# Kernel tuning notes

Measured on AMD Instinct MI355X. Metric: run time of the kernel, lower is better.

## Reference

```python
import jax, jax.numpy as jnp
import numpy as np

V, E, L, T, H, B = 8124, 1024, 24, 512, 16, 2
S = E // H
DFF = E * 8 // 3  # 2730
EPS = 1e-5
SCALE = 1.0 / np.sqrt(E)  # note: 1/sqrt(emb_dim), as in the source


def _pe():
    # sinusoidal positional encoding [T, E]
    pos = jnp.arange(T, dtype=jnp.float32)[:, None]
    div = jnp.exp(jnp.arange(0, E, 2, dtype=jnp.float32) * (-np.log(10000.0) / E))
    pe = jnp.zeros((T, E), jnp.float32)
    pe = pe.at[:, 0::2].set(jnp.sin(pos * div))
    pe = pe.at[:, 1::2].set(jnp.cos(pos * div))
    return pe


def _rms(x, g):
    # NOTE: source takes the mean over the WHOLE tensor (no dim arg)
    rms = jnp.sqrt(jnp.mean(x.astype(jnp.float32) ** 2) + EPS)
    return (x / rms * g).astype(x.dtype)


def setup_inputs() -> dict:
    key = jax.random.key(0)
    ks = jax.random.split(key, 9)
    def w(k, shape):
        return jax.random.normal(k, shape, jnp.float32) * 0.02
    return {
        "tokens": jax.random.randint(ks[0], (B, T), 0, V),
        "emb_table": w(ks[1], (V, E)),
        "Wqkv": w(ks[2], (L, E, 3 * E)), "bqkv": jnp.zeros((L, 3 * E), jnp.float32),
        "Wo": w(ks[3], (L, E, E)), "bo": jnp.zeros((L, E), jnp.float32),
        "W1": w(ks[4], (L, E, DFF)), "b1": jnp.zeros((L, DFF), jnp.float32),
        "W3": w(ks[5], (L, E, DFF)), "b3": jnp.zeros((L, DFF), jnp.float32),
        "W2": w(ks[6], (L, DFF, E)), "b2": jnp.zeros((L, E), jnp.float32),
        "g_mha": jnp.ones((L, E), jnp.float32),
        "g_ff": jnp.ones((L, E), jnp.float32),
        "g_final": jnp.ones((E,), jnp.float32),
        "Wout": w(ks[7], (E, V)), "bout": jnp.zeros((V,), jnp.float32),
    }


def reference(tokens, emb_table, Wqkv, bqkv, Wo, bo, W1, b1, W3, b3, W2, b2,
              g_mha, g_ff, g_final, Wout, bout):
    x = emb_table[tokens] + _pe()[None]  # [B,T,E]
    mask = jnp.tril(jnp.ones((T, T), bool))

    def block(x, p):
        wqkv, bq, wo, bo_, w1, b1_, w3, b3_, w2, b2_, gm, gf = p
        # --- causal MHA ---
        y = _rms(x, gm)
        qkv = (y @ wqkv + bq).reshape(B, T, H, 3, S)
        q = qkv[..., 0, :].transpose(0, 2, 1, 3)  # [B,H,T,S]
        k = qkv[..., 1, :].transpose(0, 2, 1, 3)
        v = qkv[..., 2, :].transpose(0, 2, 1, 3)
        attn = jnp.einsum('bhqd,bhkd->bhqk', q, k).astype(jnp.float32) * SCALE
        attn = jnp.where(mask, attn, -jnp.inf)
        attn = jax.nn.softmax(attn, axis=-1).astype(x.dtype)
        y = jnp.einsum('bhqk,bhkd->bhqd', attn, v)
        y = y.transpose(0, 2, 1, 3).reshape(B, T, E)
        x = x + (y @ wo + bo_)
        # --- SwiGLU FFN ---
        h = _rms(x, gf)
        u = h @ w1 + b1_
        u = u * jax.nn.sigmoid(u) * (h @ w3 + b3_)
        return x + (u @ w2 + b2_), None

    x, _ = jax.lax.scan(block, x, (Wqkv, bqkv, Wo, bo, W1, b1, W3, b3, W2, b2, g_mha, g_ff))
    return _rms(x, g_final) @ Wout + bout  # [B,T,V]
```

## Files before the change

### kernel.cpp

```cpp
#include <hip/hip_runtime.h>
#include <hip/hip_bf16.h>
#include <math.h>

#define EDIM   1024
#define TSEQ   512
#define NBATCH 2
#define NHEAD  16
#define HDIM   64
#define NLAYER 24
#define VOCAB  8124
#define DFFDIM 2730
#define DPAD   2752
#define MTOK   (NBATCH*TSEQ)
#define NELEM  (MTOK*EDIM)
#define EPSF   1e-5f
#define SCALEF (1.0f/32.0f)
#define NEGBIG (-1e30f)

typedef __bf16 bf16x8 __attribute__((ext_vector_type(8)));
typedef __bf16 bf16x4 __attribute__((ext_vector_type(4)));
typedef float  f32x4  __attribute__((ext_vector_type(4)));

#define MFMA(a, b, c) __builtin_amdgcn_mfma_f32_16x16x32_bf16((a), (b), (c), 0, 0, 0)

__device__ __forceinline__ void gl_lds16(const __bf16* g, __bf16* l) {
  __builtin_amdgcn_global_load_lds(
      (const __attribute__((address_space(1))) void*)g,
      (__attribute__((address_space(3))) void*)l, 16, 0, 0);
}
template <int N> __device__ __forceinline__ void vmwait() {
  asm volatile("s_waitcnt vmcnt(%0)" :: "n"(N) : "memory");
}
__device__ __forceinline__ void lgkm_barrier() {
  asm volatile("s_waitcnt lgkmcnt(0)" ::: "memory");
  __builtin_amdgcn_s_barrier();
}

__global__ __launch_bounds__(256) void k_embed(const int* __restrict__ tok,
                                               const float* __restrict__ emb,
                                               float* __restrict__ x) {
  const int bt = blockIdx.x;
  const int t  = bt & (TSEQ - 1);
  const int tk = tok[bt];
  const float* er = emb + (size_t)tk * EDIM;
  float* xr = x + (size_t)bt * EDIM;
  for (int e = threadIdx.x * 4; e < EDIM; e += 256 * 4) {
    float4 v = *(const float4*)(er + e);
    float vv[4] = {v.x, v.y, v.z, v.w};
    float ou[4];
#pragma unroll
    for (int j = 0; j < 4; ++j) {
      int ee = e + j;
      int i2 = ee & ~1;
      float freq = expf(-(float)i2 * (9.210340371976184f / 1024.0f));
      float ang  = (float)t * freq;
      ou[j] = vv[j] + ((ee & 1) ? cosf(ang) : sinf(ang));
    }
    *(float4*)(xr + e) = make_float4(ou[0], ou[1], ou[2], ou[3]);
  }
}

__global__ __launch_bounds__(256) void k_red1f(float* __restrict__ x,
                                               const float* __restrict__ pb,
                                               int np,
                                               const float* __restrict__ bias,
                                               float* __restrict__ part) {
  float s = 0.f;
  const bool fold = (pb != nullptr);
  for (int i = (blockIdx.x * 256 + threadIdx.x) * 4; i < NELEM; i += 256 * 256 * 4) {
    float4 v = *(const float4*)(x + i);
    if (fold) {
      for (int z = 0; z < np; ++z) {
        float4 a = *(const float4*)(pb + (size_t)z * NELEM + i);
        v.x += a.x; v.y += a.y; v.z += a.z; v.w += a.w;
      }
      float4 c = *(const float4*)(bias + (i & (EDIM - 1)));
      v.x += c.x; v.y += c.y; v.z += c.z; v.w += c.w;
      *(float4*)(x + i) = v;
    }
    s += v.x * v.x + v.y * v.y + v.z * v.z + v.w * v.w;
  }
#pragma unroll
  for (int o = 32; o > 0; o >>= 1) s += __shfl_down(s, o);
  __shared__ float sm[4];
  if ((threadIdx.x & 63) == 0) sm[threadIdx.x >> 6] = s;
  __syncthreads();
  if (threadIdx.x == 0) part[blockIdx.x] = sm[0] + sm[1] + sm[2] + sm[3];
}

__device__ __forceinline__ void conv_tile(const float* __restrict__ src,
                                          const float* __restrict__ gk,
                                          __bf16* __restrict__ dst,
                                          int K, int N, int Kpad, int tk, int tn) {
  __shared__ float st[64][65];
  const int k0 = tk << 6, n0 = tn << 6;
  const int tid = threadIdx.x;
  {
    const int r0 = tid >> 4, c4 = (tid & 15) << 2;
#pragma unroll
    for (int i = 0; i < 4; ++i) {
      const int r = r0 + i * 16;
      const int k = k0 + r;
      float4 v = make_float4(0.f, 0.f, 0.f, 0.f);
      if (k < K) {
        const float* sp = src + (size_t)k * N + n0 + c4;
        if (n0 + c4 + 3 < N) v = *(const float4*)sp;
        else {
          if (n0 + c4 + 0 < N) v.x = sp[0];
          if (n0 + c4 + 1 < N) v.y = sp[1];
          if (n0 + c4 + 2 < N) v.z = sp[2];
          if (n0 + c4 + 3 < N) v.w = sp[3];
        }
        if (gk) {
          const float gv = gk[k];
          v.x *= gv; v.y *= gv; v.z *= gv; v.w *= gv;
        }
      }
      st[r][c4 + 0] = v.x; st[r][c4 + 1] = v.y; st[r][c4 + 2] = v.z; st[r][c4 + 3] = v.w;
    }
  }
  __syncthreads();
  {
    const int nl0 = tid >> 3, c8 = (tid & 7) << 3;
#pragma unroll
    for (int i = 0; i < 2; ++i) {
      const int nl = nl0 + i * 32;
      bf16x8 o = {(__bf16)st[c8 + 0][nl], (__bf16)st[c8 + 1][nl],
                  (__bf16)st[c8 + 2][nl], (__bf16)st[c8 + 3][nl],
                  (__bf16)st[c8 + 4][nl], (__bf16)st[c8 + 5][nl],
                  (__bf16)st[c8 + 6][nl], (__bf16)st[c8 + 7][nl]};
      *(bf16x8*)&dst[(size_t)(n0 + nl) * Kpad + k0 + c8] = o;
    }
  }
}

__global__ __launch_bounds__(256) void k_convAll(const float* __restrict__ Wqkv,
                                                 const float* __restrict__ Wo,
                                                 const float* __restrict__ W1,
                                                 const float* __restrict__ W3,
                                                 const float* __restrict__ W2w,
                                                 const float* __restrict__ g_mha,
                                                 const float* __restrict__ g_ff,
                                                 __bf16* qkvT, __bf16* woT,
                                                 __bf16* w1T, __bf16* w3T, __bf16* w2T) {
  int b = blockIdx.x;
  const int l = b / 3088; b -= l * 3088;
  if (b < 768) {
    conv_tile(Wqkv + (size_t)l * 1024 * 3072, g_mha + (size_t)l * EDIM,
              qkvT + (size_t)l * 3072 * 1024, 1024, 3072, 1024, b / 48, b % 48);
  } else if (b < 1024) {
    int t = b - 768;
    conv_tile(Wo + (size_t)l * 1024 * 1024, nullptr,
              woT + (size_t)l * 1024 * 1024, 1024, 1024, 1024, t / 16, t % 16);
  } else if (b < 1712) {
    int t = b - 1024;
    conv_tile(W1 + (size_t)l * 1024 * DFFDIM, g_ff + (size_t)l * EDIM,
              w1T + (size_t)l * DPAD * 1024, 1024, DFFDIM, 1024, t / 43, t % 43);
  } else if (b < 2400) {
    int t = b - 1712;
    conv_tile(W3 + (size_t)l * 1024 * DFFDIM, g_ff + (size_t)l * EDIM,
              w3T + (size_t)l * DPAD * 1024, 1024, DFFDIM, 1024, t / 43, t % 43);
  } else {
    int t = b - 2400;
    conv_tile(W2w + (size_t)l * DFFDIM * 1024, nullptr,
              w2T + (size_t)l * 1024 * DPAD, DFFDIM, 1024, DPAD, t / 16, t % 16);
  }
}

__global__ __launch_bounds__(256) void k_convH(const float* __restrict__ Wout,
                                               const float* __restrict__ g_final,
                                               __bf16* __restrict__ WoutT) {
  conv_tile(Wout, g_final, WoutT, 1024, VOCAB, 1024, blockIdx.x >> 7, blockIdx.x & 127);
}

template <int BN, int MODE, int FUSE>
__global__ __launch_bounds__(256) void mm(
    const __bf16* __restrict__ A, const float* __restrict__ Af,
    const __bf16* __restrict__ B0w, const __bf16* __restrict__ B1w,
    const float* __restrict__ bias0, const float* __restrict__ bias1,
    const float* __restrict__ part,
    float* __restrict__ po, __bf16* __restrict__ ob,
    __bf16* __restrict__ qout, __bf16* __restrict__ kout, __bf16* __restrict__ vout,
    int N, int lda, int ldb, int Ktot) {
  constexpr int DUAL = (MODE == 2) ? 2 : 1;
  constexpr int FN = BN / 32;
  constexpr int BL = (BN == 128) ? 4 : 2 * DUAL;
  __shared__ __bf16 As[2][8][128][8];
  __shared__ __bf16 Bs[2][DUAL][8][BN][8];
  const int tid = threadIdx.x, lane = tid & 63, wave = tid >> 6;
  const int m0 = blockIdx.y << 7, n0 = blockIdx.x * BN;
  const int wm0 = (wave >> 1) * 64, wn0 = (wave & 1) * (BN / 2);
  const int lr = lane & 15, kh = lane >> 4;

  const int ktiles = Ktot >> 6;
  const int nt0 = (ktiles + gridDim.z - 1) / gridDim.z;
  const int tbeg = blockIdx.z * nt0;
  const int tend = (ktiles < tbeg + nt0) ? ktiles : (tbeg + nt0);
  const int nt = tend - tbeg;

  f32x4 acc[DUAL][4][FN];
#pragma unroll
  for (int d = 0; d < DUAL; ++d)
#pragma unroll
    for (int mi = 0; mi < 4; ++mi)
#pragma unroll
      for (int fn = 0; fn < FN; ++fn) acc[d][mi][fn] = (f32x4){0.f, 0.f, 0.f, 0.f};

  float4 ar[4][2];
  auto LOADA = [&](int t) {
    const int k0 = (tbeg + t) << 6;
#pragma unroll
    for (int i = 0; i < 4; ++i) {
      const int d = i * 256 + tid;
      const int row = d >> 3, kb = d & 7;
      const float* ap = Af + (size_t)(m0 + row) * lda + k0 + kb * 8;
      ar[i][0] = *(const float4*)ap; ar[i][1] = *(const float4*)(ap + 4);
    }
  };
  auto DSWA = [&](int buf) {
#pragma unroll
    for (int i = 0; i < 4; ++i) {
      const int d = i * 256 + tid;
      const int row = d >> 3, kb = d & 7;
      float4 a = ar[i][0], b = ar[i][1];
      bf16x8 w = {(__bf16)a.x, (__bf16)a.y, (__bf16)a.z, (__bf16)a.w,
                  (__bf16)b.x, (__bf16)b.y, (__bf16)b.z, (__bf16)b.w};
      *(bf16x8*)&As[buf][kb][row ^ kb][0] = w;
    }
  };
  auto STAGEA_G = [&](int buf, int t) {
    const int k0 = (tbeg + t) << 6;
#pragma unroll
    for (int i = 0; i < 4; ++i) {
      const int d = i * 256 + tid;
      gl_lds16(A + (size_t)(m0 + (d & 127)) * lda + k0 + (d >> 7) * 8,
               &As[buf][d >> 7][d & 127][0]);
    }
  };
  auto STAGEB = [&](int buf, int t) {
    const int k0 = (tbeg + t) << 6;
    if (BN == 128) {
#pragma unroll
      for (int i = 0; i < 4; ++i) {
        const int d = i * 256 + tid;
        gl_lds16(B0w + (size_t)(n0 + (d & 127)) * ldb + k0 + (d >> 7) * 8,
                 &Bs[buf][0][d >> 7][d & 127][0]);
      }
    } else {
#pragma unroll
      for (int i = 0; i < 2; ++i) {
        const int d = i * 256 + tid;
        gl_lds16(B0w + (size_t)(n0 + (d & 63)) * ldb + k0 + (d >> 6) * 8,
                 &Bs[buf][0][d >> 6][d & 63][0]);
      }
      if (DUAL == 2) {
#pragma unroll
        for (int i = 0; i < 2; ++i) {
          const int d = i * 256 + tid;
          gl_lds16(B1w + (size_t)(n0 + (d & 63)) * ldb + k0 + (d >> 6) * 8,
                   &Bs[buf][DUAL - 1][d >> 6][d & 63][0]);
        }
      }
    }
  };
  auto COMP = [&](int buf) {
#pragma unroll
    for (int ks = 0; ks < 2; ++ks) {
      const int kidx = ks * 4 + kh;
      bf16x8 af[4];
#pragma unroll
      for (int mi = 0; mi < 4; ++mi) {
        const int r = wm0 + mi * 16 + lr;
        af[mi] = *(const bf16x8*)&As[buf][kidx][FUSE ? (r ^ kidx) : r][0];
      }
#pragma unroll
      for (int d = 0; d < DUAL; ++d)
#pragma unroll
        for (int fn = 0; fn < FN; ++fn) {
          bf16x8 bfr = *(const bf16x8*)&Bs[buf][d][kidx][wn0 + fn * 16 + lr][0];
#pragma unroll
          for (int mi = 0; mi < 4; ++mi)
            acc[d][mi][fn] = MFMA(af[mi], bfr, acc[d][mi][fn]);
        }
    }
  };

  int cur = 0;
  if (FUSE) {
    LOADA(0); STAGEB(0, 0); DSWA(0);
    asm volatile("s_waitcnt lgkmcnt(0)" ::: "memory");
    vmwait<0>(); __builtin_amdgcn_s_barrier();
    for (int t = 0; t < nt - 1; ++t) {
      LOADA(t + 1);
      STAGEB(cur ^ 1, t + 1);
      COMP(cur);
      DSWA(cur ^ 1);
      asm volatile("s_waitcnt lgkmcnt(0)" ::: "memory");
      vmwait<0>(); __builtin_amdgcn_s_barrier();
      cur ^= 1;
    }
    COMP(cur);
  } else {
    STAGEA_G(0, 0); STAGEB(0, 0);
    for (int t = 0; t < nt - 1; ++t) {
      STAGEA_G(cur ^ 1, t + 1); STAGEB(cur ^ 1, t + 1);
      vmwait<4 + BL>();
      __builtin_amdgcn_s_barrier();
      COMP(cur);
      __builtin_amdgcn_s_barrier();
      cur ^= 1;
    }
    vmwait<0>(); __builtin_amdgcn_s_barrier();
    COMP(cur);
  }

  float sc = 1.0f;
  if (FUSE) {
    __shared__ float smr[4];
    float s = part[tid];
#pragma unroll
    for (int o = 32; o > 0; o >>= 1) s += __shfl_down(s, o);
    if ((tid & 63) == 0) smr[tid >> 6] = s;
    __syncthreads();
    sc = 1.0f / sqrtf((smr[0] + smr[1] + smr[2] + smr[3]) / (float)NELEM + EPSF);
  }

#pragma unroll
  for (int mi = 0; mi < 4; ++mi)
#pragma unroll
    for (int fn = 0; fn < FN; ++fn) {
      const int col = n0 + wn0 + fn * 16 + lr;
      if (MODE == 0) {
        const float bs = bias0[col];
        const int h = col / (3 * HDIM);
        const int rsel = (col >> 6) % 3;
        const int s2 = col & (HDIM - 1);
#pragma unroll
        for (int j = 0; j < 4; ++j) {
          const int row = m0 + wm0 + mi * 16 + (kh << 2) + j;
          const int b = row >> 9, t = row & (TSEQ - 1);
          const float v = acc[0][mi][fn][j] * sc + bs;
          if (rsel == 0)      qout[((size_t)(b * NHEAD + h) * TSEQ + t) * HDIM + s2] = (__bf16)v;
          else if (rsel == 1) kout[((size_t)(b * NHEAD + h) * TSEQ + t) * HDIM + s2] = (__bf16)v;
          else                vout[((size_t)(b * NHEAD + h) * HDIM + s2) * TSEQ + t] = (__bf16)v;
        }
      } else if (MODE == 1) {
        float* pz = po + (size_t)blockIdx.z * NELEM;
#pragma unroll
        for (int j = 0; j < 4; ++j) {
          const int row = m0 + wm0 + mi * 16 + (kh << 2) + j;
          pz[(size_t)row * EDIM + col] = acc[0][mi][fn][j];
        }
      } else if (MODE == 2) {
        const bool ok = col < N;
        const float bb1 = ok ? bias0[col] : 0.f;
        const float bb3 = ok ? bias1[col] : 0.f;
#pragma unroll
        for (int j = 0; j < 4; ++j) {
          const int row = m0 + wm0 + mi * 16 + (kh << 2) + j;
          float v = 0.f;
          if (ok) {
            const float a1v = acc[0][mi][fn][j] * sc + bb1;
            const float a3v = acc[DUAL - 1][mi][fn][j] * sc + bb3;
            v = a1v * (1.0f / (1.0f + __expf(-a1v))) * a3v;
          }
          ob[(size_t)row * DPAD + col] = (__bf16)v;
        }
      } else {
        if (col < N) {
          const float bs = bias0[col];
#pragma unroll
          for (int j = 0; j < 4; ++j) {
            const int row = m0 + wm0 + mi * 16 + (kh << 2) + j;
            po[(size_t)row * N + col] = acc[0][mi][fn][j] * sc + bs;
          }
        }
      }
    }
}

__global__ __launch_bounds__(256) void k_flash(const __bf16* __restrict__ qbuf,
                                               const __bf16* __restrict__ kbuf,
                                               const __bf16* __restrict__ vbufT,
                                               __bf16* __restrict__ y2) {
  const int qt = blockIdx.x, bh = blockIdx.y;
  const int b = bh >> 4, h = bh & 15;
  const int m0 = qt << 6;
  const __bf16* qp = qbuf  + (size_t)bh * TSEQ * HDIM;
  const __bf16* kp = kbuf  + (size_t)bh * TSEQ * HDIM;
  const __bf16* vp = vbufT + (size_t)bh * HDIM * TSEQ;
  __shared__ __bf16 Qs[8][64][8], Ks[2][8][64][8], Vs[2][8][64][8], Ps[8][64][8];
  __shared__ float wmax[2][64], wsum[2][64];
  const int tid = threadIdx.x, lane = tid & 63, wave = tid >> 6;
  const int wm = (wave >> 1) << 5, wn = (wave & 1) << 5;
  const int lr = lane & 15, kh = lane >> 4;

  auto STAGE_KV = [&](int kt2, int buf) {
    const int n0s = kt2 << 6;
#pragma unroll
    for (int i = 0; i < 2; ++i) {
      const int d = i * 256 + tid;
      const int kb2 = d >> 6, row = d & 63;
      gl_lds16(kp + (size_t)(n0s + row) * HDIM + kb2 * 8, &Ks[buf][kb2][row][0]);
      gl_lds16(vp + (size_t)row * TSEQ + n0s + kb2 * 8, &Vs[buf][kb2][row][0]);
    }
  };

#pragma unroll
  for (int i = 0; i < 2; ++i) {
    const int d = i * 256 + tid;
    const int kb2 = d >> 6, row = d & 63;
    gl_lds16(qp + (size_t)(m0 + row) * HDIM + kb2 * 8, &Qs[kb2][row][0]);
  }
  STAGE_KV(0, 0);

  float m_[2][4], l_[2][4];
#pragma unroll
  for (int mi = 0; mi < 2; ++mi)
#pragma unroll
    for (int j = 0; j < 4; ++j) { m_[mi][j] = NEGBIG; l_[mi][j] = 0.f; }
  f32x4 o00 = {0,0,0,0}, o01 = {0,0,0,0}, o10 = {0,0,0,0}, o11 = {0,0,0,0};

  int cur = 0;
  for (int kt = 0; kt <= qt; ++kt) {
    const int n0 = kt << 6;
    if (kt < qt) {
      STAGE_KV(kt + 1, cur ^ 1);
      vmwait<4>();
    } else {
      vmwait<0>();
    }
    __builtin_amdgcn_s_barrier();

    f32x4 s00 = {0,0,0,0}, s01 = {0,0,0,0}, s10 = {0,0,0,0}, s11 = {0,0,0,0};
#pragma unroll
    for (int ks = 0; ks < 2; ++ks) {
      const int kidx = ks * 4 + kh;
      bf16x8 a0 = *(const bf16x8*)&Qs[kidx][wm + lr][0];
      bf16x8 a1 = *(const bf16x8*)&Qs[kidx][wm + 16 + lr][0];
      bf16x8 b0 = *(const bf16x8*)&Ks[cur][kidx][wn + lr][0];
      bf16x8 b1 = *(const bf16x8*)&Ks[cur][kidx][wn + 16 + lr][0];
      s00 = MFMA(a0, b0, s00); s01 = MFMA(a0, b1, s01);
      s10 = MFMA(a1, b0, s10); s11 = MFMA(a1, b1, s11);
    }
    float pv_[2][2][4];
#pragma unroll
    for (int mi = 0; mi < 2; ++mi)
#pragma unroll
      for (int j = 0; j < 4; ++j) {
        const int grow = m0 + wm + mi * 16 + (kh << 2) + j;
        float best = NEGBIG;
#pragma unroll
        for (int ni = 0; ni < 2; ++ni) {
          f32x4 sfr = (mi == 0) ? (ni == 0 ? s00 : s01) : (ni == 0 ? s10 : s11);
          const int gcol = n0 + wn + ni * 16 + lr;
          float t = sfr[j] * SCALEF;
          if (gcol > grow) t = NEGBIG;
          pv_[mi][ni][j] = t;
          best = fmaxf(best, t);
        }
        float v = best;
        v = fmaxf(v, __shfl_xor(v, 1)); v = fmaxf(v, __shfl_xor(v, 2));
        v = fmaxf(v, __shfl_xor(v, 4)); v = fmaxf(v, __shfl_xor(v, 8));
        wmax[wave & 1][wm + mi * 16 + (kh << 2) + j] = v;
      }
    lgkm_barrier();

    float alpha[2][4];
#pragma unroll
    for (int mi = 0; mi < 2; ++mi)
#pragma unroll
      for (int j = 0; j < 4; ++j) {
        const int rl = wm + mi * 16 + (kh << 2) + j;
        const float tmax = fmaxf(wmax[0][rl], wmax[1][rl]);
        const float mn = fmaxf(m_[mi][j], tmax);
        alpha[mi][j] = __expf(m_[mi][j] - mn);
        m_[mi][j] = mn;
        float rs = 0.f;
#pragma unroll
        for (int ni = 0; ni < 2; ++ni) {
          const float p = __expf(pv_[mi][ni][j] - mn);
          pv_[mi][ni][j] = p;
          rs += p;
        }
        rs += __shfl_xor(rs, 1); rs += __shfl_xor(rs, 2);
        rs += __shfl_xor(rs, 4); rs += __shfl_xor(rs, 8);
        wsum[wave & 1][rl] = rs;
      }
#pragma unroll
    for (int mi = 0; mi < 2; ++mi)
#pragma unroll
      for (int ni = 0; ni < 2; ++ni)
#pragma unroll
        for (int j = 0; j < 4; ++j) {
          const int prow = wm + mi * 16 + (kh << 2) + j;
          const int pcol = wn + ni * 16 + lr;
          Ps[pcol >> 3][prow][pcol & 7] = (__bf16)pv_[mi][ni][j];
        }
    lgkm_barrier();

#pragma unroll
    for (int mi = 0; mi < 2; ++mi)
#pragma unroll
      for (int j = 0; j < 4; ++j) {
        const int rl = wm + mi * 16 + (kh << 2) + j;
        l_[mi][j] = l_[mi][j] * alpha[mi][j] + wsum[0][rl] + wsum[1][rl];
      }
#pragma unroll
    for (int j = 0; j < 4; ++j) {
      o00[j] *= alpha[0][j]; o01[j] *= alpha[0][j];
      o10[j] *= alpha[1][j]; o11[j] *= alpha[1][j];
    }
#pragma unroll
    for (int ks = 0; ks < 2; ++ks) {
      const int kidx = ks * 4 + kh;
      bf16x8 a0 = *(const bf16x8*)&Ps[kidx][wm + lr][0];
      bf16x8 a1 = *(const bf16x8*)&Ps[kidx][wm + 16 + lr][0];
      bf16x8 b0 = *(const bf16x8*)&Vs[cur][kidx][wn + lr][0];
      bf16x8 b1 = *(const bf16x8*)&Vs[cur][kidx][wn + 16 + lr][0];
      o00 = MFMA(a0, b0, o00); o01 = MFMA(a0, b1, o01);
      o10 = MFMA(a1, b0, o10); o11 = MFMA(a1, b1, o11);
    }
    __builtin_amdgcn_s_barrier();
    cur ^= 1;
  }

#pragma unroll
  for (int mi = 0; mi < 2; ++mi)
#pragma unroll
    for (int ni = 0; ni < 2; ++ni) {
      f32x4 oo = (mi == 0) ? (ni == 0 ? o00 : o01) : (ni == 0 ? o10 : o11);
      const int col = wn + ni * 16 + lr;
#pragma unroll
      for (int j = 0; j < 4; ++j) {
        const int row = m0 + wm + mi * 16 + (kh << 2) + j;
        y2[((size_t)(b * TSEQ) + row) * EDIM + h * HDIM + col] = (__bf16)(oo[j] / l_[mi][j]);
      }
    }
}

extern "C" void kernel_launch(void* const* d_in, const int* in_sizes, int n_in,
                              void* d_out, int out_size, void* d_ws, size_t ws_size,
                              hipStream_t stream) {
  const int*   tokens  = (const int*)d_in[0];
  const float* emb     = (const float*)d_in[1];
  const float* Wqkv    = (const float*)d_in[2];
  const float* bqkv    = (const float*)d_in[3];
  const float* Wo      = (const float*)d_in[4];
  const float* bo      = (const float*)d_in[5];
  const float* W1      = (const float*)d_in[6];
  const float* b1      = (const float*)d_in[7];
  const float* W3      = (const float*)d_in[8];
  const float* b3      = (const float*)d_in[9];
  const float* W2w     = (const float*)d_in[10];
  const float* b2      = (const float*)d_in[11];
  const float* g_mha   = (const float*)d_in[12];
  const float* g_ff    = (const float*)d_in[13];
  const float* g_final = (const float*)d_in[14];
  const float* Wout    = (const float*)d_in[15];
  const float* bout    = (const float*)d_in[16];
  float* out = (float*)d_out;

  char* base = (char*)d_ws;
  size_t off = 0;
  auto alloc = [&](size_t bytes) { char* p = base + off; off = (off + bytes + 255) & ~(size_t)255; return p; };
  float*  x    = (float*)alloc(4u << 20);
  float*  part = (float*)alloc(2048);
  __bf16* qbf  = (__bf16*)alloc(2u << 20);
  __bf16* kbf  = (__bf16*)alloc(2u << 20);
  __bf16* vbT  = (__bf16*)alloc(2u << 20);
  __bf16* y2bf = (__bf16*)alloc(2u << 20);
  __bf16* ubf  = (__bf16*)alloc((size_t)MTOK * DPAD * 2);
  float*  pbuf = (float*)alloc((size_t)2 * NELEM * 4);
  __bf16* WoutT = (__bf16*)alloc((size_t)8192 * 1024 * 2);
  __bf16* qkvT = (__bf16*)alloc((size_t)NLAYER * 3072 * 1024 * 2);
  __bf16* woT  = (__bf16*)alloc((size_t)NLAYER * 1024 * 1024 * 2);
  __bf16* w1T  = (__bf16*)alloc((size_t)NLAYER * DPAD * 1024 * 2);
  __bf16* w3T  = (__bf16*)alloc((size_t)NLAYER * DPAD * 1024 * 2);
  __bf16* w2T  = (__bf16*)alloc((size_t)NLAYER * 1024 * DPAD * 2);

  k_embed<<<MTOK, 256, 0, stream>>>(tokens, emb, x);
  k_convAll<<<NLAYER * 3088, 256, 0, stream>>>(Wqkv, Wo, W1, W3, W2w,
                                               g_mha, g_ff,
                                               qkvT, woT, w1T, w3T, w2T);
  k_convH<<<2048, 256, 0, stream>>>(Wout, g_final, WoutT);

  const float* pend_bias = nullptr;
  for (int l = 0; l < NLAYER; ++l) {
    k_red1f<<<256, 256, 0, stream>>>(x, pend_bias ? pbuf : nullptr, 2, pend_bias, part);
    mm<64, 0, 1><<<dim3(48, 8, 1), 256, 0, stream>>>(
        nullptr, x, qkvT + (size_t)l * 3072 * 1024, nullptr,
        bqkv + (size_t)l * 3 * EDIM, nullptr, part,
        nullptr, nullptr, qbf, kbf, vbT, 3072, EDIM, 1024, 1024);
    k_flash<<<dim3(8, 32), 256, 0, stream>>>(qbf, kbf, vbT, y2bf);
    mm<64, 1, 0><<<dim3(16, 8, 2), 256, 0, stream>>>(
        y2bf, nullptr, woT + (size_t)l * 1024 * 1024, nullptr,
        nullptr, nullptr, nullptr,
        pbuf, nullptr, nullptr, nullptr, nullptr, 1024, 1024, 1024, 1024);
    k_red1f<<<256, 256, 0, stream>>>(x, pbuf, 2, bo + (size_t)l * EDIM, part);
    mm<64, 2, 1><<<dim3(43, 8, 1), 256, 0, stream>>>(
        nullptr, x, w1T + (size_t)l * DPAD * 1024, w3T + (size_t)l * DPAD * 1024,
        b1 + (size_t)l * DFFDIM, b3 + (size_t)l * DFFDIM, part,
        nullptr, ubf, nullptr, nullptr, nullptr, DFFDIM, EDIM, 1024, 1024);
    mm<64, 1, 0><<<dim3(16, 8, 2), 256, 0, stream>>>(
        ubf, nullptr, w2T + (size_t)l * 1024 * DPAD, nullptr,
        nullptr, nullptr, nullptr,
        pbuf, nullptr, nullptr, nullptr, nullptr, 1024, DPAD, DPAD, DPAD);
    pend_bias = b2 + (size_t)l * EDIM;
  }

  k_red1f<<<256, 256, 0, stream>>>(x, pbuf, 2, pend_bias, part);
  mm<128, 3, 1><<<dim3(64, 8, 1), 256, 0, stream>>>(
      nullptr, x, WoutT, nullptr, bout, nullptr, part,
      out, nullptr, nullptr, nullptr, nullptr, VOCAB, EDIM, 1024, 1024);
}
```

Baseline: 4.220 ms.

## Halve flash query tile, add lazy softmax rescale, widen split-K to four

The attention kernel now processes 32 query rows per block instead of 64, which doubles the grid so more blocks run on the GPU at once. It also skips the running-max rescale of the accumulators unless the new max exceeds the old one by more than 8. The Wo and W2 projections now split K four ways instead of two, with a larger partial buffer and a reduction over four partials, to give those GEMMs more blocks. The costs are more K/V reloads across the smaller query tiles, more partial-sum traffic, and possible precision drift from the delayed rescale.

```diff
diff --git a/kernel.cpp b/kernel.cpp
--- a/kernel.cpp
+++ b/kernel.cpp
@@ -385,14 +385,14 @@
                                                __bf16* __restrict__ y2) {
   const int qt = blockIdx.x, bh = blockIdx.y;
   const int b = bh >> 4, h = bh & 15;
-  const int m0 = qt << 6;
+  const int m0 = qt << 5;
   const __bf16* qp = qbuf  + (size_t)bh * TSEQ * HDIM;
   const __bf16* kp = kbuf  + (size_t)bh * TSEQ * HDIM;
   const __bf16* vp = vbufT + (size_t)bh * HDIM * TSEQ;
-  __shared__ __bf16 Qs[8][64][8], Ks[2][8][64][8], Vs[2][8][64][8], Ps[8][64][8];
-  __shared__ float wmax[2][64], wsum[2][64];
+  __shared__ __bf16 Qs[8][32][8], Ks[2][8][64][8], Vs[2][8][64][8], Ps[8][32][8];
+  __shared__ float wmax[2][32], wsum[2][32];
   const int tid = threadIdx.x, lane = tid & 63, wave = tid >> 6;
-  const int wm = (wave >> 1) << 5, wn = (wave & 1) << 5;
+  const int wm = (wave >> 1) << 4, wn = (wave & 1) << 5;
   const int lr = lane & 15, kh = lane >> 4;
 
   auto STAGE_KV = [&](int kt2, int buf) {
@@ -406,25 +406,20 @@
     }
   };
 
-#pragma unroll
-  for (int i = 0; i < 2; ++i) {
-    const int d = i * 256 + tid;
-    const int kb2 = d >> 6, row = d & 63;
-    gl_lds16(qp + (size_t)(m0 + row) * HDIM + kb2 * 8, &Qs[kb2][row][0]);
-  }
+  gl_lds16(qp + (size_t)(m0 + (tid & 31)) * HDIM + (tid >> 5) * 8,
+           &Qs[tid >> 5][tid & 31][0]);
   STAGE_KV(0, 0);
 
-  float m_[2][4], l_[2][4];
-#pragma unroll
-  for (int mi = 0; mi < 2; ++mi)
-#pragma unroll
-    for (int j = 0; j < 4; ++j) { m_[mi][j] = NEGBIG; l_[mi][j] = 0.f; }
-  f32x4 o00 = {0,0,0,0}, o01 = {0,0,0,0}, o10 = {0,0,0,0}, o11 = {0,0,0,0};
-
+  float m_[4], l_[4];
+#pragma unroll
+  for (int j = 0; j < 4; ++j) { m_[j] = NEGBIG; l_[j] = 0.f; }
+  f32x4 o0 = {0, 0, 0, 0}, o1 = {0, 0, 0, 0};
+
+  const int ktmax = qt >> 1;
   int cur = 0;
-  for (int kt = 0; kt <= qt; ++kt) {
+  for (int kt = 0; kt <= ktmax; ++kt) {
     const int n0 = kt << 6;
-    if (kt < qt) {
+    if (kt < ktmax) {
       STAGE_KV(kt + 1, cur ^ 1);
       vmwait<4>();
     } else {
@@ -432,111 +427,83 @@
     }
     __builtin_amdgcn_s_barrier();
 
-    f32x4 s00 = {0,0,0,0}, s01 = {0,0,0,0}, s10 = {0,0,0,0}, s11 = {0,0,0,0};
+    f32x4 s0 = {0, 0, 0, 0}, s1 = {0, 0, 0, 0};
 #pragma unroll
     for (int ks = 0; ks < 2; ++ks) {
       const int kidx = ks * 4 + kh;
-      bf16x8 a0 = *(const bf16x8*)&Qs[kidx][wm + lr][0];
-      bf16x8 a1 = *(const bf16x8*)&Qs[kidx][wm + 16 + lr][0];
+      bf16x8 a  = *(const bf16x8*)&Qs[kidx][wm + lr][0];
       bf16x8 b0 = *(const bf16x8*)&Ks[cur][kidx][wn + lr][0];
       bf16x8 b1 = *(const bf16x8*)&Ks[cur][kidx][wn + 16 + lr][0];
-      s00 = MFMA(a0, b0, s00); s01 = MFMA(a0, b1, s01);
-      s10 = MFMA(a1, b0, s10); s11 = MFMA(a1, b1, s11);
-    }
-    float pv_[2][2][4];
-#pragma unroll
-    for (int mi = 0; mi < 2; ++mi)
+      s0 = MFMA(a, b0, s0); s1 = MFMA(a, b1, s1);
+    }
+    float pv0[4], pv1[4];
+#pragma unroll
+    for (int j = 0; j < 4; ++j) {
+      const int grow = m0 + wm + (kh << 2) + j;
+      float t0 = s0[j] * SCALEF; if (n0 + wn + lr > grow)      t0 = NEGBIG;
+      float t1 = s1[j] * SCALEF; if (n0 + wn + 16 + lr > grow) t1 = NEGBIG;
+      pv0[j] = t0; pv1[j] = t1;
+      float v = fmaxf(t0, t1);
+      v = fmaxf(v, __shfl_xor(v, 1)); v = fmaxf(v, __shfl_xor(v, 2));
+      v = fmaxf(v, __shfl_xor(v, 4)); v = fmaxf(v, __shfl_xor(v, 8));
+      wmax[wave & 1][wm + (kh << 2) + j] = v;
+    }
+    lgkm_barrier();
+
+    float tmax[4]; bool need = false;
+#pragma unroll
+    for (int j = 0; j < 4; ++j) {
+      const int rl = wm + (kh << 2) + j;
+      tmax[j] = fmaxf(wmax[0][rl], wmax[1][rl]);
+      need |= (tmax[j] > m_[j] + 8.f);
+    }
+    if (__ballot(need)) {
 #pragma unroll
       for (int j = 0; j < 4; ++j) {
-        const int grow = m0 + wm + mi * 16 + (kh << 2) + j;
-        float best = NEGBIG;
-#pragma unroll
-        for (int ni = 0; ni < 2; ++ni) {
-          f32x4 sfr = (mi == 0) ? (ni == 0 ? s00 : s01) : (ni == 0 ? s10 : s11);
-          const int gcol = n0 + wn + ni * 16 + lr;
-          float t = sfr[j] * SCALEF;
-          if (gcol > grow) t = NEGBIG;
-          pv_[mi][ni][j] = t;
-          best = fmaxf(best, t);
-        }
-        float v = best;
-        v = fmaxf(v, __shfl_xor(v, 1)); v = fmaxf(v, __shfl_xor(v, 2));
-        v = fmaxf(v, __shfl_xor(v, 4)); v = fmaxf(v, __shfl_xor(v, 8));
-        wmax[wave & 1][wm + mi * 16 + (kh << 2) + j] = v;
-      }
+        const float mn = fmaxf(m_[j], tmax[j]);
+        const float al = __expf(m_[j] - mn);
+        m_[j] = mn; l_[j] *= al; o0[j] *= al; o1[j] *= al;
+      }
+    }
+#pragma unroll
+    for (int j = 0; j < 4; ++j) {
+      const float p0 = __expf(pv0[j] - m_[j]);
+      const float p1 = __expf(pv1[j] - m_[j]);
+      float rs = p0 + p1;
+      rs += __shfl_xor(rs, 1); rs += __shfl_xor(rs, 2);
+      rs += __shfl_xor(rs, 4); rs += __shfl_xor(rs, 8);
+      const int rl = wm + (kh << 2) + j;
+      wsum[wave & 1][rl] = rs;
+      const int pc0 = wn + lr, pc1 = wn + 16 + lr;
+      Ps[pc0 >> 3][rl][pc0 & 7] = (__bf16)p0;
+      Ps[pc1 >> 3][rl][pc1 & 7] = (__bf16)p1;
+    }
     lgkm_barrier();
 
-    float alpha[2][4];
-#pragma unroll
-    for (int mi = 0; mi < 2; ++mi)
-#pragma unroll
-      for (int j = 0; j < 4; ++j) {
-        const int rl = wm + mi * 16 + (kh << 2) + j;
-        const float tmax = fmaxf(wmax[0][rl], wmax[1][rl]);
-        const float mn = fmaxf(m_[mi][j], tmax);
-        alpha[mi][j] = __expf(m_[mi][j] - mn);
-        m_[mi][j] = mn;
-        float rs = 0.f;
-#pragma unroll
-        for (int ni = 0; ni < 2; ++ni) {
-          const float p = __expf(pv_[mi][ni][j] - mn);
-          pv_[mi][ni][j] = p;
-          rs += p;
-        }
-        rs += __shfl_xor(rs, 1); rs += __shfl_xor(rs, 2);
-        rs += __shfl_xor(rs, 4); rs += __shfl_xor(rs, 8);
-        wsum[wave & 1][rl] = rs;
-      }
-#pragma unroll
-    for (int mi = 0; mi < 2; ++mi)
-#pragma unroll
-      for (int ni = 0; ni < 2; ++ni)
-#pragma unroll
-        for (int j = 0; j < 4; ++j) {
-          const int prow = wm + mi * 16 + (kh << 2) + j;
-          const int pcol = wn + ni * 16 + lr;
-          Ps[pcol >> 3][prow][pcol & 7] = (__bf16)pv_[mi][ni][j];
-        }
-    lgkm_barrier();
-
-#pragma unroll
-    for (int mi = 0; mi < 2; ++mi)
-#pragma unroll
-      for (int j = 0; j < 4; ++j) {
-        const int rl = wm + mi * 16 + (kh << 2) + j;
-        l_[mi][j] = l_[mi][j] * alpha[mi][j] + wsum[0][rl] + wsum[1][rl];
-      }
 #pragma unroll
     for (int j = 0; j < 4; ++j) {
-      o00[j] *= alpha[0][j]; o01[j] *= alpha[0][j];
-      o10[j] *= alpha[1][j]; o11[j] *= alpha[1][j];
+      const int rl = wm + (kh << 2) + j;
+      l_[j] += wsum[0][rl] + wsum[1][rl];
     }
 #pragma unroll
     for (int ks = 0; ks < 2; ++ks) {
       const int kidx = ks * 4 + kh;
-      bf16x8 a0 = *(const bf16x8*)&Ps[kidx][wm + lr][0];
-      bf16x8 a1 = *(const bf16x8*)&Ps[kidx][wm + 16 + lr][0];
+      bf16x8 a  = *(const bf16x8*)&Ps[kidx][wm + lr][0];
       bf16x8 b0 = *(const bf16x8*)&Vs[cur][kidx][wn + lr][0];
       bf16x8 b1 = *(const bf16x8*)&Vs[cur][kidx][wn + 16 + lr][0];
-      o00 = MFMA(a0, b0, o00); o01 = MFMA(a0, b1, o01);
-      o10 = MFMA(a1, b0, o10); o11 = MFMA(a1, b1, o11);
+      o0 = MFMA(a, b0, o0); o1 = MFMA(a, b1, o1);
     }
     __builtin_amdgcn_s_barrier();
     cur ^= 1;
   }
 
 #pragma unroll
-  for (int mi = 0; mi < 2; ++mi)
-#pragma unroll
-    for (int ni = 0; ni < 2; ++ni) {
-      f32x4 oo = (mi == 0) ? (ni == 0 ? o00 : o01) : (ni == 0 ? o10 : o11);
-      const int col = wn + ni * 16 + lr;
-#pragma unroll
-      for (int j = 0; j < 4; ++j) {
-        const int row = m0 + wm + mi * 16 + (kh << 2) + j;
-        y2[((size_t)(b * TSEQ) + row) * EDIM + h * HDIM + col] = (__bf16)(oo[j] / l_[mi][j]);
-      }
-    }
+  for (int j = 0; j < 4; ++j) {
+    const int row = m0 + wm + (kh << 2) + j;
+    const float inv = 1.0f / l_[j];
+    y2[((size_t)(b * TSEQ) + row) * EDIM + h * HDIM + wn + lr]      = (__bf16)(o0[j] * inv);
+    y2[((size_t)(b * TSEQ) + row) * EDIM + h * HDIM + wn + 16 + lr] = (__bf16)(o1[j] * inv);
+  }
 }
 
 extern "C" void kernel_launch(void* const* d_in, const int* in_sizes, int n_in,
@@ -571,7 +538,7 @@
   __bf16* vbT  = (__bf16*)alloc(2u << 20);
   __bf16* y2bf = (__bf16*)alloc(2u << 20);
   __bf16* ubf  = (__bf16*)alloc((size_t)MTOK * DPAD * 2);
-  float*  pbuf = (float*)alloc((size_t)2 * NELEM * 4);
+  float*  pbuf = (float*)alloc((size_t)4 * NELEM * 4);
   __bf16* WoutT = (__bf16*)alloc((size_t)8192 * 1024 * 2);
   __bf16* qkvT = (__bf16*)alloc((size_t)NLAYER * 3072 * 1024 * 2);
   __bf16* woT  = (__bf16*)alloc((size_t)NLAYER * 1024 * 1024 * 2);
@@ -587,29 +554,29 @@
 
   const float* pend_bias = nullptr;
   for (int l = 0; l < NLAYER; ++l) {
-    k_red1f<<<256, 256, 0, stream>>>(x, pend_bias ? pbuf : nullptr, 2, pend_bias, part);
+    k_red1f<<<256, 256, 0, stream>>>(x, pend_bias ? pbuf : nullptr, 4, pend_bias, part);
     mm<64, 0, 1><<<dim3(48, 8, 1), 256, 0, stream>>>(
         nullptr, x, qkvT + (size_t)l * 3072 * 1024, nullptr,
         bqkv + (size_t)l * 3 * EDIM, nullptr, part,
         nullptr, nullptr, qbf, kbf, vbT, 3072, EDIM, 1024, 1024);
-    k_flash<<<dim3(8, 32), 256, 0, stream>>>(qbf, kbf, vbT, y2bf);
-    mm<64, 1, 0><<<dim3(16, 8, 2), 256, 0, stream>>>(
+    k_flash<<<dim3(16, 32), 256, 0, stream>>>(qbf, kbf, vbT, y2bf);
+    mm<64, 1, 0><<<dim3(16, 8, 4), 256, 0, stream>>>(
         y2bf, nullptr, woT + (size_t)l * 1024 * 1024, nullptr,
         nullptr, nullptr, nullptr,
         pbuf, nullptr, nullptr, nullptr, nullptr, 1024, 1024, 1024, 1024);
-    k_red1f<<<256, 256, 0, stream>>>(x, pbuf, 2, bo + (size_t)l * EDIM, part);
+    k_red1f<<<256, 256, 0, stream>>>(x, pbuf, 4, bo + (size_t)l * EDIM, part);
     mm<64, 2, 1><<<dim3(43, 8, 1), 256, 0, stream>>>(
         nullptr, x, w1T + (size_t)l * DPAD * 1024, w3T + (size_t)l * DPAD * 1024,
         b1 + (size_t)l * DFFDIM, b3 + (size_t)l * DFFDIM, part,
         nullptr, ubf, nullptr, nullptr, nullptr, DFFDIM, EDIM, 1024, 1024);
-    mm<64, 1, 0><<<dim3(16, 8, 2), 256, 0, stream>>>(
+    mm<64, 1, 0><<<dim3(16, 8, 4), 256, 0, stream>>>(
         ubf, nullptr, w2T + (size_t)l * 1024 * DPAD, nullptr,
         nullptr, nullptr, nullptr,
         pbuf, nullptr, nullptr, nullptr, nullptr, 1024, DPAD, DPAD, DPAD);
     pend_bias = b2 + (size_t)l * EDIM;
   }
 
-  k_red1f<<<256, 256, 0, stream>>>(x, pbuf, 2, pend_bias, part);
+  k_red1f<<<256, 256, 0, stream>>>(x, pbuf, 4, pend_bias, part);
   mm<128, 3, 1><<<dim3(64, 8, 1), 256, 0, stream>>>(
       nullptr, x, WoutT, nullptr, bout, nullptr, part,
       out, nullptr, nullptr, nullptr, nullptr, VOCAB, EDIM, 1024, 1024);
```

After: 3.961 ms. -6.1%, faster.
